# Kernel tuning notes

Hardware: AMD Instinct MI355X
Metric: run time of the kernel (lower is better)

Reference implementation:

```python
import jax, jax.numpy as jnp
import numpy as np

INV_SQRT2 = 0.7071067811865476  # 1/sqrt(2), matches pywt db1 dec filters
LEVEL = 3  # init_kwargs level


def setup_inputs() -> dict:
    key = jax.random.key(0)
    x = jax.random.normal(key, (64, 64, 8192), dtype=jnp.float32)
    return {"x": x}


def reference(x):
    # Wavelet packet transform, wavelet='db1' (Haar), level=3, mode='symmetric'.
    # For Haar with even-length inputs, symmetric padding has no effect and the
    # pywt coefficients are exactly pairwise scaled sums/differences.
    # Natural-order nodes at the final level correspond to stacking [approx, detail]
    # children at every split (path a->0, d->1, binary order).
    B, C, S = x.shape
    nodes = x[:, :, None, :]  # [B, C, n_nodes=1, len=S]
    for _ in range(LEVEL):
        even = nodes[..., 0::2]
        odd = nodes[..., 1::2]
        a = (even + odd) * INV_SQRT2  # lowpass + downsample
        d = (even - odd) * INV_SQRT2  # highpass + downsample
        # children in natural order: [a, d] per parent node
        k = nodes.shape[2]
        nodes = jnp.stack([a, d], axis=3).reshape(B, C, 2 * k, -1)
    # flatten the 2^LEVEL nodes per channel, as the original np flatten does
    return nodes.reshape(B, C, S)
```

## Files before the change

### kernel.cpp

```cpp
#include <hip/hip_runtime.h>


#define C3 0.35355339059327373f

__global__ __launch_bounds__(256) void swpt3_kernel(const float4* __restrict__ x,
                                                    float* __restrict__ out) {
    __shared__ float lds[1024];

    const unsigned t   = threadIdx.x;
    const unsigned b   = blockIdx.x;
    const unsigned row = b >> 3;
    const unsigned ch  = b & 7u;

    const float4 v = x[(size_t)row * 2048u + ch * 256u + t];

    const float s0 = v.x + v.y, d0 = v.x - v.y;
    const float s1 = v.z + v.w, d1 = v.z - v.w;
    const float e0 = s0 + s1;
    const float e2 = s0 - s1;
    const float e4 = d0 + d1;
    const float e6 = d0 - d1;

    const int p = (int)(t & 1u);
    const float f0 = __shfl_xor(e0, 1);
    const float f2 = __shfl_xor(e2, 1);
    const float f4 = __shfl_xor(e4, 1);
    const float f6 = __shfl_xor(e6, 1);

    const float a0 = p ? -e0 : e0;
    const float a2 = p ? -e2 : e2;
    const float a4 = p ? -e4 : e4;
    const float a6 = p ? -e6 : e6;
    const float r0 = (f0 + a0) * C3;
    const float r2 = (f2 + a2) * C3;
    const float r4 = (f4 + a4) * C3;
    const float r6 = (f6 + a6) * C3;

    const unsigned j = t >> 1;
    lds[(0u + p) * 128u + j] = r0;
    lds[(2u + p) * 128u + j] = r2;
    lds[(4u + p) * 128u + j] = r4;
    lds[(6u + p) * 128u + j] = r6;

    __syncthreads();

    const float4 r = ((const float4*)lds)[t];
    const unsigned n = t >> 5;
    const unsigned m = t & 31u;
    float4* o = (float4*)(out + (size_t)row * 8192u + n * 1024u + ch * 128u + 4u * m);
    *o = r;
}

extern "C" void kernel_launch(void* const* d_in, const int* in_sizes, int n_in,
                              void* d_out, int out_size, void* d_ws, size_t ws_size,
                              hipStream_t stream) {
    const float4* x = (const float4*)d_in[0];
    float* out = (float*)d_out;
    swpt3_kernel<<<32768, 256, 0, stream>>>(x, out);
}
```

Baseline: 218.2 us.

## Compute full 8-point Haar group per thread, drop LDS and shuffles

```diff
diff --git a/kernel.cpp b/kernel.cpp
--- a/kernel.cpp
+++ b/kernel.cpp
@@ -5,50 +5,39 @@
 
 __global__ __launch_bounds__(256) void swpt3_kernel(const float4* __restrict__ x,
                                                     float* __restrict__ out) {
-    __shared__ float lds[1024];
+    const unsigned g = blockIdx.x * 256u + threadIdx.x;
 
-    const unsigned t   = threadIdx.x;
-    const unsigned b   = blockIdx.x;
-    const unsigned row = b >> 3;
-    const unsigned ch  = b & 7u;
+    const float4 va = x[(size_t)g * 2u];
+    const float4 vb = x[(size_t)g * 2u + 1u];
 
-    const float4 v = x[(size_t)row * 2048u + ch * 256u + t];
+    const float s0 = va.x + va.y, d0 = va.x - va.y;
+    const float s1 = va.z + va.w, d1 = va.z - va.w;
+    const float s2 = vb.x + vb.y, d2 = vb.x - vb.y;
+    const float s3 = vb.z + vb.w, d3 = vb.z - vb.w;
+    const float ss0 = s0 + s1, sd0 = s0 - s1;
+    const float ss1 = s2 + s3, sd1 = s2 - s3;
+    const float ds0 = d0 + d1, dd0 = d0 - d1;
+    const float ds1 = d2 + d3, dd1 = d2 - d3;
+    const float r0 = (ss0 + ss1) * C3;
+    const float r1 = (ss0 - ss1) * C3;
+    const float r2 = (sd0 + sd1) * C3;
+    const float r3 = (sd0 - sd1) * C3;
+    const float r4 = (ds0 + ds1) * C3;
+    const float r5 = (ds0 - ds1) * C3;
+    const float r6 = (dd0 + dd1) * C3;
+    const float r7 = (dd0 - dd1) * C3;
 
-    const float s0 = v.x + v.y, d0 = v.x - v.y;
-    const float s1 = v.z + v.w, d1 = v.z - v.w;
-    const float e0 = s0 + s1;
-    const float e2 = s0 - s1;
-    const float e4 = d0 + d1;
-    const float e6 = d0 - d1;
-
-    const int p = (int)(t & 1u);
-    const float f0 = __shfl_xor(e0, 1);
-    const float f2 = __shfl_xor(e2, 1);
-    const float f4 = __shfl_xor(e4, 1);
-    const float f6 = __shfl_xor(e6, 1);
-
-    const float a0 = p ? -e0 : e0;
-    const float a2 = p ? -e2 : e2;
-    const float a4 = p ? -e4 : e4;
-    const float a6 = p ? -e6 : e6;
-    const float r0 = (f0 + a0) * C3;
-    const float r2 = (f2 + a2) * C3;
-    const float r4 = (f4 + a4) * C3;
-    const float r6 = (f6 + a6) * C3;
-
-    const unsigned j = t >> 1;
-    lds[(0u + p) * 128u + j] = r0;
-    lds[(2u + p) * 128u + j] = r2;
-    lds[(4u + p) * 128u + j] = r4;
-    lds[(6u + p) * 128u + j] = r6;
-
-    __syncthreads();
-
-    const float4 r = ((const float4*)lds)[t];
-    const unsigned n = t >> 5;
-    const unsigned m = t & 31u;
-    float4* o = (float4*)(out + (size_t)row * 8192u + n * 1024u + ch * 128u + 4u * m);
-    *o = r;
+    const unsigned row = g >> 10;
+    const unsigned j   = g & 1023u;
+    float* o = out + (size_t)row * 8192u + j;
+    o[0]        = r0;
+    o[1024u]    = r1;
+    o[2048u]    = r2;
+    o[3072u]    = r3;
+    o[4096u]    = r4;
+    o[5120u]    = r5;
+    o[6144u]    = r6;
+    o[7168u]    = r7;
 }
 
 extern "C" void kernel_launch(void* const* d_in, const int* in_sizes, int n_in,
@@ -56,5 +45,5 @@
                               hipStream_t stream) {
     const float4* x = (const float4*)d_in[0];
     float* out = (float*)d_out;
-    swpt3_kernel<<<32768, 256, 0, stream>>>(x, out);
+    swpt3_kernel<<<16384, 256, 0, stream>>>(x, out);
 }
```

Result: slower. 226.6 us (+3.9%).

## Process half-rows per wavefront with prefetched loop and wave-local LDS transpose

Applied to the files above, without the earlier changes.

```diff
diff --git a/kernel.cpp b/kernel.cpp
--- a/kernel.cpp
+++ b/kernel.cpp
@@ -6,49 +6,67 @@
 __global__ __launch_bounds__(256) void swpt3_kernel(const float4* __restrict__ x,
                                                     float* __restrict__ out) {
     __shared__ float lds[1024];
+    const unsigned tid  = threadIdx.x;
+    const unsigned lane = tid & 63u;
+    const unsigned wid  = tid >> 6;
 
-    const unsigned t   = threadIdx.x;
-    const unsigned b   = blockIdx.x;
-    const unsigned row = b >> 3;
-    const unsigned ch  = b & 7u;
+    float* W = lds + (wid << 8);
 
-    const float4 v = x[(size_t)row * 2048u + ch * 256u + t];
+    const unsigned gw   = blockIdx.x * 4u + wid;
+    const unsigned row  = gw >> 1;
+    const unsigned half = gw & 1u;
 
-    const float s0 = v.x + v.y, d0 = v.x - v.y;
-    const float s1 = v.z + v.w, d1 = v.z - v.w;
-    const float e0 = s0 + s1;
-    const float e2 = s0 - s1;
-    const float e4 = d0 + d1;
-    const float e6 = d0 - d1;
+    const float4* xh = x + (size_t)row * 2048u + (size_t)half * 1024u + lane;
+    float* orow = out + (size_t)row * 8192u;
 
-    const int p = (int)(t & 1u);
-    const float f0 = __shfl_xor(e0, 1);
-    const float f2 = __shfl_xor(e2, 1);
-    const float f4 = __shfl_xor(e4, 1);
-    const float f6 = __shfl_xor(e6, 1);
+    const unsigned p  = lane & 1u;
+    const unsigned jl = lane >> 1;
 
-    const float a0 = p ? -e0 : e0;
-    const float a2 = p ? -e2 : e2;
-    const float a4 = p ? -e4 : e4;
-    const float a6 = p ? -e6 : e6;
-    const float r0 = (f0 + a0) * C3;
-    const float r2 = (f2 + a2) * C3;
-    const float r4 = (f4 + a4) * C3;
-    const float r6 = (f6 + a6) * C3;
+    float* w0 = W + p * 32u + jl;
+    const float4* rd = (const float4*)W + lane;
+    float* ob = orow + (lane >> 3) * 1024u + half * 512u + 4u * (lane & 7u);
 
-    const unsigned j = t >> 1;
-    lds[(0u + p) * 128u + j] = r0;
-    lds[(2u + p) * 128u + j] = r2;
-    lds[(4u + p) * 128u + j] = r4;
-    lds[(6u + p) * 128u + j] = r6;
+    float4 v0 = xh[0];
+    float4 v1 = xh[64];
 
-    __syncthreads();
+    #pragma unroll
+    for (unsigned i = 0; i < 16; ++i) {
+        float4 vn = v1;
+        if (i + 2u < 16u) vn = xh[(i + 2u) * 64u];
 
-    const float4 r = ((const float4*)lds)[t];
-    const unsigned n = t >> 5;
-    const unsigned m = t & 31u;
-    float4* o = (float4*)(out + (size_t)row * 8192u + n * 1024u + ch * 128u + 4u * m);
-    *o = r;
+        const float s0 = v0.x + v0.y, d0 = v0.x - v0.y;
+        const float s1 = v0.z + v0.w, d1 = v0.z - v0.w;
+        const float e0 = s0 + s1;
+        const float e2 = s0 - s1;
+        const float e4 = d0 + d1;
+        const float e6 = d0 - d1;
+
+        const float f0 = __shfl_xor(e0, 1);
+        const float f2 = __shfl_xor(e2, 1);
+        const float f4 = __shfl_xor(e4, 1);
+        const float f6 = __shfl_xor(e6, 1);
+
+        const float r0 = (f0 + (p ? -e0 : e0)) * C3;
+        const float r2 = (f2 + (p ? -e2 : e2)) * C3;
+        const float r4 = (f4 + (p ? -e4 : e4)) * C3;
+        const float r6 = (f6 + (p ? -e6 : e6)) * C3;
+
+        w0[0]   = r0;
+        w0[64]  = r2;
+        w0[128] = r4;
+        w0[192] = r6;
+
+        __builtin_amdgcn_wave_barrier();
+
+        const float4 r = *rd;
+
+        __builtin_amdgcn_wave_barrier();
+
+        *(float4*)(ob + i * 32u) = r;
+
+        v0 = v1;
+        v1 = vn;
+    }
 }
 
 extern "C" void kernel_launch(void* const* d_in, const int* in_sizes, int n_in,
@@ -56,5 +74,5 @@
                               hipStream_t stream) {
     const float4* x = (const float4*)d_in[0];
     float* out = (float*)d_out;
-    swpt3_kernel<<<32768, 256, 0, stream>>>(x, out);
+    swpt3_kernel<<<2048, 256, 0, stream>>>(x, out);
 }
```

After: 233.9 us. 7.2% more time.
